# Optimization experiments

Hardware: AMD Instinct MI355X
Metric: run time of the kernel (lower is better)

Reference implementation:

```python
import jax, jax.numpy as jnp
import numpy as np

OUT, IN = 5632, 2048
GROUP_SIZE = 128
N_GROUPS = (OUT * IN) // GROUP_SIZE
LORA_SCALE = 32.0 / 16.0  # lora_alpha / lora_r


def dequantize_int4(packed, scales, zeros):
    # packed: [numel//2], each byte holds two 4-bit codes (low nibble first)
    low = packed & 0xF
    high = (packed >> 4) & 0xF
    q = jnp.stack([low, high], axis=-1).reshape(-1).astype(jnp.float32)  # [numel]
    q = q.reshape(N_GROUPS, GROUP_SIZE)
    w = (q - zeros[:, None]) * scales[:, None]
    return w.reshape(OUT, IN)


def setup_inputs() -> dict:
    key = jax.random.key(0)
    k1, k2, k3, k4, k5, k6 = jax.random.split(key, 6)
    x = jax.random.normal(k1, (4, 2048, IN), dtype=jnp.float32)
    packed = jax.random.randint(k2, ((OUT * IN) // 2,), 0, 256, dtype=jnp.int32)
    scales = jax.random.uniform(k3, (N_GROUPS,), dtype=jnp.float32) * 0.02 + 1e-3
    zeros = jax.random.uniform(k4, (N_GROUPS,), dtype=jnp.float32) * 15.0
    lora_A = jax.random.normal(k5, (IN, 16), dtype=jnp.float32) * (1.0 / np.sqrt(IN))
    lora_B = jax.random.normal(k6, (16, OUT), dtype=jnp.float32) * 0.02
    return {"x": x, "packed": packed, "scales": scales, "zeros": zeros,
            "lora_A": lora_A, "lora_B": lora_B}


def reference(x, packed, scales, zeros, lora_A, lora_B):
    W = dequantize_int4(packed, scales, zeros)            # [OUT, IN]
    base = jnp.einsum('bsi,oi->bso', x, W)                # F.linear(x, W)
    lora = ((x @ lora_A) @ lora_B) * LORA_SCALE           # low-rank path
    return base + lora
```

## Files before the change

kernel.cpp:

```cpp
#include <hip/hip_runtime.h>

#define M_DIM 8192
#define K_DIM 2048
#define N_DIM 5632

typedef __attribute__((ext_vector_type(8))) short short8;
typedef __attribute__((ext_vector_type(4))) short s4v;
typedef __attribute__((ext_vector_type(4))) float f32x4;

__device__ __forceinline__ short f2b(float f) {
  union { float f; unsigned u; } v; v.f = f;
  unsigned r = v.u + 0x7FFFu + ((v.u >> 16) & 1u);
  return (short)(r >> 16);
}

__device__ __forceinline__ void async16(void* lds, const void* g) {
  __builtin_amdgcn_global_load_lds(
      (const __attribute__((address_space(1))) unsigned*)g,
      (__attribute__((address_space(3))) unsigned*)lds,
      16, 0, 0);
}

__global__ __launch_bounds__(256) void cvt_x_kernel(const float* __restrict__ x,
                                                    short* __restrict__ xb) {
  long t = (long)blockIdx.x * 256 + threadIdx.x;
  float4 f = ((const float4*)x)[t];
  s4v o;
  o[0] = f2b(f.x); o[1] = f2b(f.y); o[2] = f2b(f.z); o[3] = f2b(f.w);
  *(s4v*)(xb + 4 * t) = o;
}

__global__ __launch_bounds__(256) void lat_kernel(const float* __restrict__ lA,
                                                  float* __restrict__ lAT) {
  int i = blockIdx.x * 256 + threadIdx.x;
  const float4* row = (const float4*)(lA + (size_t)i * 16);
  float4 v0 = row[0], v1 = row[1], v2 = row[2], v3 = row[3];
  float vals[16] = {v0.x, v0.y, v0.z, v0.w, v1.x, v1.y, v1.z, v1.w,
                    v2.x, v2.y, v2.z, v2.w, v3.x, v3.y, v3.z, v3.w};
#pragma unroll
  for (int r = 0; r < 16; ++r) lAT[r * K_DIM + i] = vals[r] * 2.0f;
}

__global__ __launch_bounds__(256) void dequant_lora_kernel(
    const int* __restrict__ packed, const float* __restrict__ scales,
    const float* __restrict__ zeros, const float* __restrict__ lAT,
    const float* __restrict__ lB, short* __restrict__ wb) {
  int o = blockIdx.x;
  int i0 = threadIdx.x * 8;
  long e0 = (long)o * K_DIM + i0;
  int4 p = ((const int4*)packed)[e0 >> 3];
  int g = (int)(e0 >> 7);
  float s = scales[g], z = zeros[g];

  float accv[8];
#pragma unroll
  for (int d = 0; d < 4; ++d) {
    int pv = (&p.x)[d];
    accv[2 * d]     = ((float)(pv & 0xF) - z) * s;
    accv[2 * d + 1] = ((float)((pv >> 4) & 0xF) - z) * s;
  }
#pragma unroll
  for (int r = 0; r < 16; ++r) {
    float b = lB[r * N_DIM + o];
    const float4* ar = (const float4*)&lAT[r * K_DIM + i0];
    float4 a0 = ar[0], a1 = ar[1];
    accv[0] += a0.x * b; accv[1] += a0.y * b;
    accv[2] += a0.z * b; accv[3] += a0.w * b;
    accv[4] += a1.x * b; accv[5] += a1.y * b;
    accv[6] += a1.z * b; accv[7] += a1.w * b;
  }
  short8 out8;
#pragma unroll
  for (int j = 0; j < 8; ++j) out8[j] = f2b(accv[j]);
  *(short8*)(wb + e0) = out8;
}

__global__ __launch_bounds__(512, 2) void gemm_kernel(const short* __restrict__ xb,
                                                      const short* __restrict__ wb,
                                                      float* __restrict__ out) {
  __shared__ __align__(16) short lds[65536];

  const int tid = threadIdx.x;
  const int lane = tid & 63;
  const int wave = tid >> 6;
  const int wm = wave >> 2, wn = wave & 3;
  const int l15 = lane & 15, quad = lane >> 4;

  int flat = blockIdx.x;
  int swz = (flat & 7) * 88 + (flat >> 3);
  int bm = swz / 22, bn_ = swz - bm * 22;
  const int m0 = bm * 256, n0 = bn_ * 256;

  const short* a_base = xb + (size_t)m0 * K_DIM;
  const short* b_base = wb + (size_t)n0 * K_DIM;

  const int rswz = quad ^ ((l15 >> 1) & 3);
  const int a_rd = (wm * 128 + l15) * 32 + rswz * 8;
  const int b_rd = (wn * 64 + l15) * 32 + rswz * 8;

  const int srow = tid >> 2;
  const int schunk = (tid & 3) ^ ((srow >> 1) & 3);
  const short* ag0 = a_base + (size_t)srow * K_DIM + schunk * 8;
  const short* bg0 = b_base + (size_t)srow * K_DIM + schunk * 8;
  const int sl0 = tid * 8, sl1 = (512 + tid) * 8;

  f32x4 acc[8][4] = {};

  auto stageA = [&](int t, int s) {
    const int d = (t & 1) * 16384 + s * 8192;
    const short* g = ag0 + t * 64 + s * 32;
    async16(&lds[d + sl0], g);
    async16(&lds[d + sl1], g + (size_t)128 * K_DIM);
  };
  auto stageB = [&](int t, int s) {
    const int d = 32768 + (t & 1) * 16384 + s * 8192;
    const short* g = bg0 + t * 64 + s * 32;
    async16(&lds[d + sl0], g);
    async16(&lds[d + sl1], g + (size_t)128 * K_DIM);
  };

  stageA(0, 0); stageB(0, 0);
  stageA(0, 1); stageB(0, 1);
  asm volatile("s_waitcnt vmcnt(4)" ::: "memory");
  __builtin_amdgcn_s_barrier();

  auto tile = [&](int t, bool st, int vm1, int vm3) {
    const int cb = (t & 1) * 16384;
    short8 af[4], bf[4];
#pragma unroll
    for (int n = 0; n < 4; ++n) bf[n] = *(const short8*)&lds[32768 + cb + b_rd + n * 512];
#pragma unroll
    for (int m = 0; m < 4; ++m) af[m] = *(const short8*)&lds[cb + a_rd + m * 512];
    if (st) stageA(t + 1, 0);
    __builtin_amdgcn_s_barrier();
    asm volatile("s_waitcnt lgkmcnt(0)" ::: "memory");
    __builtin_amdgcn_sched_barrier(0);
    __builtin_amdgcn_s_setprio(1);
#pragma unroll
    for (int m = 0; m < 4; ++m)
#pragma unroll
      for (int n = 0; n < 4; ++n)
        acc[m][n] = __builtin_amdgcn_mfma_f32_16x16x32_bf16(af[m], bf[n], acc[m][n], 0, 0, 0);
    __builtin_amdgcn_s_setprio(0);
    __builtin_amdgcn_s_barrier();
#pragma unroll
    for (int m = 0; m < 4; ++m) af[m] = *(const short8*)&lds[cb + a_rd + (4 + m) * 512];
    if (st) stageB(t + 1, 0);
    __builtin_amdgcn_s_barrier();
    asm volatile("s_waitcnt lgkmcnt(0)" ::: "memory");
    __builtin_amdgcn_sched_barrier(0);
    __builtin_amdgcn_s_setprio(1);
#pragma unroll
    for (int m = 0; m < 4; ++m)
#pragma unroll
      for (int n = 0; n < 4; ++n)
        acc[4 + m][n] = __builtin_amdgcn_mfma_f32_16x16x32_bf16(af[m], bf[n], acc[4 + m][n], 0, 0, 0);
    __builtin_amdgcn_s_setprio(0);
    if (vm1 == 4) asm volatile("s_waitcnt vmcnt(4)" ::: "memory");
    else if (vm1 == 0) asm volatile("s_waitcnt vmcnt(0)" ::: "memory");
    __builtin_amdgcn_s_barrier();
#pragma unroll
    for (int n = 0; n < 4; ++n) bf[n] = *(const short8*)&lds[32768 + cb + 8192 + b_rd + n * 512];
#pragma unroll
    for (int m = 0; m < 4; ++m) af[m] = *(const short8*)&lds[cb + 8192 + a_rd + m * 512];
    if (st) stageA(t + 1, 1);
    __builtin_amdgcn_s_barrier();
    asm volatile("s_waitcnt lgkmcnt(0)" ::: "memory");
    __builtin_amdgcn_sched_barrier(0);
    __builtin_amdgcn_s_setprio(1);
#pragma unroll
    for (int m = 0; m < 4; ++m)
#pragma unroll
      for (int n = 0; n < 4; ++n)
        acc[m][n] = __builtin_amdgcn_mfma_f32_16x16x32_bf16(af[m], bf[n], acc[m][n], 0, 0, 0);
    __builtin_amdgcn_s_setprio(0);
    __builtin_amdgcn_s_barrier();
#pragma unroll
    for (int m = 0; m < 4; ++m) af[m] = *(const short8*)&lds[cb + 8192 + a_rd + (4 + m) * 512];
    if (st) stageB(t + 1, 1);
    __builtin_amdgcn_s_barrier();
    asm volatile("s_waitcnt lgkmcnt(0)" ::: "memory");
    __builtin_amdgcn_sched_barrier(0);
    __builtin_amdgcn_s_setprio(1);
#pragma unroll
    for (int m = 0; m < 4; ++m)
#pragma unroll
      for (int n = 0; n < 4; ++n)
        acc[4 + m][n] = __builtin_amdgcn_mfma_f32_16x16x32_bf16(af[m], bf[n], acc[4 + m][n], 0, 0, 0);
    __builtin_amdgcn_s_setprio(0);
    if (vm3 == 4) asm volatile("s_waitcnt vmcnt(4)" ::: "memory");
    else if (vm3 == 0) asm volatile("s_waitcnt vmcnt(0)" ::: "memory");
    __builtin_amdgcn_s_barrier();
  };

#pragma unroll 1
  for (int t = 0; t < 31; ++t) tile(t, true, 4, 4);
  tile(31, false, 0, -1);

  float* op = out + (size_t)(m0 + wm * 128 + quad * 4) * N_DIM + n0 + wn * 64 + l15;
#pragma unroll
  for (int mi = 0; mi < 8; ++mi)
#pragma unroll
    for (int r = 0; r < 4; ++r)
#pragma unroll
      for (int ni = 0; ni < 4; ++ni)
        op[(size_t)(mi * 16 + r) * N_DIM + ni * 16] = acc[mi][ni][r];
}

extern "C" void kernel_launch(void* const* d_in, const int* in_sizes, int n_in,
                              void* d_out, int out_size, void* d_ws, size_t ws_size,
                              hipStream_t stream) {
  const float* x      = (const float*)d_in[0];
  const int*   packed = (const int*)d_in[1];
  const float* scales = (const float*)d_in[2];
  const float* zeros  = (const float*)d_in[3];
  const float* lA     = (const float*)d_in[4];
  const float* lB     = (const float*)d_in[5];
  float* out = (float*)d_out;

  short* xb = (short*)d_ws;
  short* wb = xb + (size_t)M_DIM * K_DIM;
  float* lAT = out + ((size_t)4 * 2048 * N_DIM - 16 * K_DIM);

  cvt_x_kernel<<<(M_DIM * K_DIM) / (256 * 4), 256, 0, stream>>>(x, xb);
  lat_kernel<<<K_DIM / 256, 256, 0, stream>>>(lA, lAT);
  dequant_lora_kernel<<<N_DIM, 256, 0, stream>>>(packed, scales, zeros, lAT, lB, wb);
  gemm_kernel<<<dim3(N_DIM / 256 * (M_DIM / 256)), 512, 0, stream>>>(xb, wb, out);
}
```

Before: 465.0 us.

## Software-pipeline GEMM LDS fragment loads with register double buffering and fewer barriers

Rewrites the GEMM main loop so A/B fragments are double-buffered in registers (afX/afY, bfP/bfQ). Each LDS read for the next MFMA group is issued before the current group runs, with partial lgkmcnt waits instead of full drains. Block barriers per K-tile drop from eight to two, and the next tile's first fragments are prefetched at the end of each iteration. The aim is to hide LDS latency and barrier stalls behind MFMA work. In exchange it uses more VGPRs and depends on hand-tuned waitcnt counts being correct for the async global-to-LDS copies.

```diff
diff --git a/kernel.cpp b/kernel.cpp
--- a/kernel.cpp
+++ b/kernel.cpp
@@ -105,6 +105,7 @@
   const int sl0 = tid * 8, sl1 = (512 + tid) * 8;
 
   f32x4 acc[8][4] = {};
+  short8 afX[4], afY[4], bfP[4], bfQ[4];
 
   auto stageA = [&](int t, int s) {
     const int d = (t & 1) * 16384 + s * 8192;
@@ -118,84 +119,75 @@
     async16(&lds[d + sl0], g);
     async16(&lds[d + sl1], g + (size_t)128 * K_DIM);
   };
+  auto mm4 = [&](int base, short8* a4, short8* b4) {
+#pragma unroll
+    for (int m = 0; m < 4; ++m)
+#pragma unroll
+      for (int n = 0; n < 4; ++n)
+        acc[base + m][n] = __builtin_amdgcn_mfma_f32_16x16x32_bf16(
+            a4[m], b4[n], acc[base + m][n], 0, 0, 0);
+  };
 
   stageA(0, 0); stageB(0, 0);
   stageA(0, 1); stageB(0, 1);
   asm volatile("s_waitcnt vmcnt(4)" ::: "memory");
   __builtin_amdgcn_s_barrier();
-
-  auto tile = [&](int t, bool st, int vm1, int vm3) {
+#pragma unroll
+  for (int n = 0; n < 4; ++n) bfP[n] = *(const short8*)&lds[32768 + b_rd + n * 512];
+#pragma unroll
+  for (int m = 0; m < 4; ++m) afX[m] = *(const short8*)&lds[a_rd + m * 512];
+
+#pragma unroll 1
+  for (int t = 0; t < 32; ++t) {
     const int cb = (t & 1) * 16384;
-    short8 af[4], bf[4];
-#pragma unroll
-    for (int n = 0; n < 4; ++n) bf[n] = *(const short8*)&lds[32768 + cb + b_rd + n * 512];
-#pragma unroll
-    for (int m = 0; m < 4; ++m) af[m] = *(const short8*)&lds[cb + a_rd + m * 512];
+    const int nb = ((t + 1) & 1) * 16384;
+    const bool st = (t < 31);
+#pragma unroll
+    for (int m = 0; m < 4; ++m) afY[m] = *(const short8*)&lds[cb + a_rd + (4 + m) * 512];
     if (st) stageA(t + 1, 0);
+    asm volatile("s_waitcnt lgkmcnt(4)" ::: "memory");
+    __builtin_amdgcn_sched_barrier(0);
+    __builtin_amdgcn_s_setprio(1);
+    mm4(0, afX, bfP);
+    __builtin_amdgcn_s_setprio(0);
+    if (st) asm volatile("s_waitcnt vmcnt(2)" ::: "memory");
+    else    asm volatile("s_waitcnt vmcnt(0)" ::: "memory");
     __builtin_amdgcn_s_barrier();
-    asm volatile("s_waitcnt lgkmcnt(0)" ::: "memory");
-    __builtin_amdgcn_sched_barrier(0);
-    __builtin_amdgcn_s_setprio(1);
-#pragma unroll
-    for (int m = 0; m < 4; ++m)
-#pragma unroll
-      for (int n = 0; n < 4; ++n)
-        acc[m][n] = __builtin_amdgcn_mfma_f32_16x16x32_bf16(af[m], bf[n], acc[m][n], 0, 0, 0);
-    __builtin_amdgcn_s_setprio(0);
+#pragma unroll
+    for (int n = 0; n < 4; ++n) bfQ[n] = *(const short8*)&lds[32768 + cb + 8192 + b_rd + n * 512];
+#pragma unroll
+    for (int m = 0; m < 4; ++m) afX[m] = *(const short8*)&lds[cb + 8192 + a_rd + m * 512];
+    if (st) stageB(t + 1, 0);
+    asm volatile("s_waitcnt lgkmcnt(8)" ::: "memory");
+    __builtin_amdgcn_sched_barrier(0);
+    __builtin_amdgcn_s_setprio(1);
+    mm4(4, afY, bfP);
+    __builtin_amdgcn_s_setprio(0);
+#pragma unroll
+    for (int m = 0; m < 4; ++m) afY[m] = *(const short8*)&lds[cb + 8192 + a_rd + (4 + m) * 512];
+    if (st) stageA(t + 1, 1);
+    asm volatile("s_waitcnt lgkmcnt(4)" ::: "memory");
+    __builtin_amdgcn_sched_barrier(0);
+    __builtin_amdgcn_s_setprio(1);
+    mm4(0, afX, bfQ);
+    __builtin_amdgcn_s_setprio(0);
+    if (st) asm volatile("s_waitcnt vmcnt(2)" ::: "memory");
     __builtin_amdgcn_s_barrier();
-#pragma unroll
-    for (int m = 0; m < 4; ++m) af[m] = *(const short8*)&lds[cb + a_rd + (4 + m) * 512];
-    if (st) stageB(t + 1, 0);
-    __builtin_amdgcn_s_barrier();
-    asm volatile("s_waitcnt lgkmcnt(0)" ::: "memory");
-    __builtin_amdgcn_sched_barrier(0);
-    __builtin_amdgcn_s_setprio(1);
-#pragma unroll
-    for (int m = 0; m < 4; ++m)
-#pragma unroll
-      for (int n = 0; n < 4; ++n)
-        acc[4 + m][n] = __builtin_amdgcn_mfma_f32_16x16x32_bf16(af[m], bf[n], acc[4 + m][n], 0, 0, 0);
-    __builtin_amdgcn_s_setprio(0);
-    if (vm1 == 4) asm volatile("s_waitcnt vmcnt(4)" ::: "memory");
-    else if (vm1 == 0) asm volatile("s_waitcnt vmcnt(0)" ::: "memory");
-    __builtin_amdgcn_s_barrier();
-#pragma unroll
-    for (int n = 0; n < 4; ++n) bf[n] = *(const short8*)&lds[32768 + cb + 8192 + b_rd + n * 512];
-#pragma unroll
-    for (int m = 0; m < 4; ++m) af[m] = *(const short8*)&lds[cb + 8192 + a_rd + m * 512];
-    if (st) stageA(t + 1, 1);
-    __builtin_amdgcn_s_barrier();
-    asm volatile("s_waitcnt lgkmcnt(0)" ::: "memory");
-    __builtin_amdgcn_sched_barrier(0);
-    __builtin_amdgcn_s_setprio(1);
-#pragma unroll
-    for (int m = 0; m < 4; ++m)
-#pragma unroll
-      for (int n = 0; n < 4; ++n)
-        acc[m][n] = __builtin_amdgcn_mfma_f32_16x16x32_bf16(af[m], bf[n], acc[m][n], 0, 0, 0);
-    __builtin_amdgcn_s_setprio(0);
-    __builtin_amdgcn_s_barrier();
-#pragma unroll
-    for (int m = 0; m < 4; ++m) af[m] = *(const short8*)&lds[cb + 8192 + a_rd + (4 + m) * 512];
-    if (st) stageB(t + 1, 1);
-    __builtin_amdgcn_s_barrier();
-    asm volatile("s_waitcnt lgkmcnt(0)" ::: "memory");
-    __builtin_amdgcn_sched_barrier(0);
-    __builtin_amdgcn_s_setprio(1);
-#pragma unroll
-    for (int m = 0; m < 4; ++m)
-#pragma unroll
-      for (int n = 0; n < 4; ++n)
-        acc[4 + m][n] = __builtin_amdgcn_mfma_f32_16x16x32_bf16(af[m], bf[n], acc[4 + m][n], 0, 0, 0);
-    __builtin_amdgcn_s_setprio(0);
-    if (vm3 == 4) asm volatile("s_waitcnt vmcnt(4)" ::: "memory");
-    else if (vm3 == 0) asm volatile("s_waitcnt vmcnt(0)" ::: "memory");
-    __builtin_amdgcn_s_barrier();
-  };
-
-#pragma unroll 1
-  for (int t = 0; t < 31; ++t) tile(t, true, 4, 4);
-  tile(31, false, 0, -1);
+    if (st) {
+#pragma unroll
+      for (int n = 0; n < 4; ++n) bfP[n] = *(const short8*)&lds[32768 + nb + b_rd + n * 512];
+#pragma unroll
+      for (int m = 0; m < 4; ++m) afX[m] = *(const short8*)&lds[nb + a_rd + m * 512];
+      stageB(t + 1, 1);
+      asm volatile("s_waitcnt lgkmcnt(8)" ::: "memory");
+    } else {
+      asm volatile("s_waitcnt lgkmcnt(0)" ::: "memory");
+    }
+    __builtin_amdgcn_sched_barrier(0);
+    __builtin_amdgcn_s_setprio(1);
+    mm4(4, afY, bfQ);
+    __builtin_amdgcn_s_setprio(0);
+  }
 
   float* op = out + (size_t)(m0 + wm * 128 + quad * 4) * N_DIM + n0 + wn * 64 + l15;
 #pragma unroll
```

Result: faster. 452.7 us (-2.7%).
